# Kernel tuning notes

Measured on AMD Instinct MI355X. Metric: run time of the kernel, lower is better.

## Reference

```python
import jax, jax.numpy as jnp
import numpy as np

D_MODEL = 1024
NUM_HEADS = 16


def setup_inputs() -> dict:
    key = jax.random.key(0)
    kx, kq, kk, kv, ko = jax.random.split(key, 5)
    B, S, D = 4, 2048, D_MODEL
    scale = 0.02
    x = jax.random.normal(kx, (B, S, D), dtype=jnp.float32)
    wq = jax.random.normal(kq, (D, D), dtype=jnp.float32) * scale
    wk = jax.random.normal(kk, (D, D), dtype=jnp.float32) * scale
    wv = jax.random.normal(kv, (D, D), dtype=jnp.float32) * scale
    wo = jax.random.normal(ko, (D, D), dtype=jnp.float32) * scale
    return {"x": x, "wq": wq, "wk": wk, "wv": wv, "wo": wo}


def reference(x, wq, wk, wv, wo):
    B, S, D = x.shape
    H = NUM_HEADS
    dk = D // H
    # projections: weight is [out, in] -> y = x @ W^T
    q = jnp.einsum('bsd,ed->bse', x, wq).reshape(B, S, H, dk).transpose(0, 2, 1, 3)
    k = jnp.einsum('bsd,ed->bse', x, wk).reshape(B, S, H, dk).transpose(0, 2, 1, 3)
    v = jnp.einsum('bsd,ed->bse', x, wv).reshape(B, S, H, dk).transpose(0, 2, 1, 3)
    # scaled dot-product attention with causal mask, [B,H,S,S]
    scores = jnp.einsum('bhqd,bhkd->bhqk', q, k) / jnp.sqrt(jnp.asarray(dk, x.dtype))
    causal = jnp.tril(jnp.ones((S, S), dtype=bool))
    scores = jnp.where(causal, scores, -jnp.inf)
    attn = jax.nn.softmax(scores, axis=-1)
    out = jnp.einsum('bhqk,bhkd->bhqd', attn, v)
    out = out.transpose(0, 2, 1, 3).reshape(B, S, D)
    return jnp.einsum('bse,de->bsd', out, wo)
```

## Files before the change

### kernel.cpp

```cpp
#include <hip/hip_runtime.h>

#define SEQ 2048
#define DM 1024
#define NH 16
#define DKH 64

typedef __attribute__((ext_vector_type(8))) short short8;
typedef __attribute__((ext_vector_type(4))) float f32x4;

static __device__ __forceinline__ unsigned short f2b(float f) {
  unsigned int u = __float_as_uint(f);
  u += 0x7fffu + ((u >> 16) & 1u);
  return (unsigned short)(u >> 16);
}

static __device__ __forceinline__ short8 ldfrag_bf(const unsigned short* p) {
  return *reinterpret_cast<const short8*>(p);
}
static __device__ __forceinline__ short8 ldfrag_f32(const float* p) {
  const float4* q = reinterpret_cast<const float4*>(p);
  float4 a = q[0], b = q[1];
  short8 r;
  r[0] = (short)f2b(a.x); r[1] = (short)f2b(a.y);
  r[2] = (short)f2b(a.z); r[3] = (short)f2b(a.w);
  r[4] = (short)f2b(b.x); r[5] = (short)f2b(b.y);
  r[6] = (short)f2b(b.z); r[7] = (short)f2b(b.w);
  return r;
}

static __device__ __forceinline__ void gl_lds16(const void* g, void* l) {
  __builtin_amdgcn_global_load_lds(
      (const __attribute__((address_space(1))) unsigned int*)g,
      (__attribute__((address_space(3))) unsigned int*)l, 16, 0, 0);
}

__global__ __launch_bounds__(256) void zero_f32(float* __restrict__ p, int n4) {
  int i = blockIdx.x * 256 + threadIdx.x;
  if (i < n4) {
    float4 z = {0.f, 0.f, 0.f, 0.f};
    reinterpret_cast<float4*>(p)[i] = z;
  }
}

__global__ __launch_bounds__(256) void cast_f32_bf16(const float* __restrict__ src,
                                                     unsigned short* __restrict__ dst,
                                                     int n4) {
  int i = blockIdx.x * 256 + threadIdx.x;
  if (i < n4) {
    float4 v = reinterpret_cast<const float4*>(src)[i];
    ushort4 o;
    o.x = f2b(v.x); o.y = f2b(v.y); o.z = f2b(v.z); o.w = f2b(v.w);
    reinterpret_cast<ushort4*>(dst)[i] = o;
  }
}

__global__ __launch_bounds__(256) void cast4_w(const float* __restrict__ a, const float* __restrict__ b,
                                               const float* __restrict__ c, const float* __restrict__ d,
                                               unsigned short* __restrict__ oa, unsigned short* __restrict__ ob,
                                               unsigned short* __restrict__ oc, unsigned short* __restrict__ od) {
  int which = blockIdx.x >> 10;
  int i = (blockIdx.x & 1023) * 256 + threadIdx.x;
  const float* s = (which == 0) ? a : (which == 1) ? b : (which == 2) ? c : d;
  unsigned short* o = (which == 0) ? oa : (which == 1) ? ob : (which == 2) ? oc : od;
  float sc = (which == 0) ? 0.125f : 1.0f;
  float4 v = reinterpret_cast<const float4*>(s)[i];
  ushort4 u;
  u.x = f2b(v.x * sc); u.y = f2b(v.y * sc); u.z = f2b(v.z * sc); u.w = f2b(v.w * sc);
  reinterpret_cast<ushort4*>(o)[i] = u;
}

__global__ __launch_bounds__(256) void gemm_qkv(const unsigned short* __restrict__ A,
                                                const unsigned short* __restrict__ Wq,
                                                const unsigned short* __restrict__ Wk,
                                                const unsigned short* __restrict__ Wv,
                                                unsigned short* __restrict__ Qb,
                                                unsigned short* __restrict__ Kb,
                                                unsigned short* __restrict__ Vt) {
  __shared__ char smem[32768];
  unsigned short* At = (unsigned short*)smem;
  unsigned short* Wt = (unsigned short*)(smem + 16384);
  int t = threadIdx.x;
  int lane = t & 63;
  int w = t >> 6;
  int l16 = lane & 15, q4 = lane >> 4;
  int mode = blockIdx.x % 3;
  int bid = blockIdx.x / 3;
  int mt = bid >> 3, nt = bid & 7;
  int m0 = mt * 128, n0 = nt * 128;
  int mw = (w & 1) * 64, nw = (w >> 1) * 64;
  const unsigned short* W = (mode == 0) ? Wq : (mode == 1) ? Wk : Wv;

  const f32x4 zero4 = {0.f, 0.f, 0.f, 0.f};
  f32x4 acc[4][4];
#pragma unroll
  for (int mi = 0; mi < 4; ++mi)
#pragma unroll
    for (int nj = 0; nj < 4; ++nj) acc[mi][nj] = zero4;

  int rl0 = t >> 2, cp = t & 3;
  const unsigned short* ga0 = A + (long)(m0 + rl0) * DM + ((cp - rl0) & 3) * 8;
  const unsigned short* ga1 = A + (long)(m0 + rl0 + 64) * DM + ((cp - (rl0 + 64)) & 3) * 8;
  const unsigned short* gw0 = W + (long)(n0 + rl0) * DM + ((cp - rl0) & 3) * 8;
  const unsigned short* gw1 = W + (long)(n0 + rl0 + 64) * DM + ((cp - (rl0 + 64)) & 3) * 8;
  char* lA = (char*)At + t * 16;
  char* lW = (char*)Wt + t * 16;

  int aoff[4], woff[4];
#pragma unroll
  for (int mi = 0; mi < 4; ++mi) {
    int r = mw + mi * 16 + l16;
    aoff[mi] = r * 32 + ((q4 + r) & 3) * 8;
  }
#pragma unroll
  for (int nj = 0; nj < 4; ++nj) {
    int r = nw + nj * 16 + l16;
    woff[nj] = r * 32 + ((q4 + r) & 3) * 8;
  }

  gl_lds16(ga0, lA); gl_lds16(ga1, lA + 4096);
  gl_lds16(gw0, lW); gl_lds16(gw1, lW + 4096);

  for (int ks = 0; ks < 32; ++ks) {
    __syncthreads();
    if (ks + 1 < 32) {
      ga0 += 32; ga1 += 32; gw0 += 32; gw1 += 32;
      int bo = ((ks + 1) & 1) * 8192;
      gl_lds16(ga0, lA + bo); gl_lds16(ga1, lA + bo + 4096);
      gl_lds16(gw0, lW + bo); gl_lds16(gw1, lW + bo + 4096);
    }
    const unsigned short* Ab = At + (ks & 1) * 4096;
    const unsigned short* Wb = Wt + (ks & 1) * 4096;

    short8 af[4], wf[4];
#pragma unroll
    for (int mi = 0; mi < 4; ++mi) af[mi] = ldfrag_bf(Ab + aoff[mi]);
#pragma unroll
    for (int nj = 0; nj < 4; ++nj) wf[nj] = ldfrag_bf(Wb + woff[nj]);
#pragma unroll
    for (int mi = 0; mi < 4; ++mi)
#pragma unroll
      for (int nj = 0; nj < 4; ++nj)
        acc[mi][nj] = __builtin_amdgcn_mfma_f32_16x16x32_bf16(af[mi], wf[nj], acc[mi][nj], 0, 0, 0);
  }

  if (mode != 2) {
    unsigned short* o = (mode == 0) ? Qb : Kb;
#pragma unroll
    for (int mi = 0; mi < 4; ++mi)
#pragma unroll
      for (int nj = 0; nj < 4; ++nj)
#pragma unroll
        for (int r = 0; r < 4; ++r) {
          int m = m0 + mw + mi * 16 + q4 * 4 + r;
          int n = n0 + nw + nj * 16 + l16;
          int b = m >> 11, s = m & 2047;
          int h = n >> 6, d = n & 63;
          long bh = (long)(b * NH + h);
          o[(bh * SEQ + s) * DKH + d] = f2b(acc[mi][nj][r]);
        }
  } else {
    __syncthreads();
    unsigned short* vle = (unsigned short*)(smem + w * 8192);
    unsigned int* vle32 = (unsigned int*)vle;
#pragma unroll
    for (int nj = 0; nj < 4; ++nj) {
      int d = nj * 16 + l16;
      int k8 = (d & 7) * 8;
#pragma unroll
      for (int mi = 0; mi < 4; ++mi)
#pragma unroll
        for (int r = 0; r < 4; r += 2) {
          int s = mi * 16 + q4 * 4 + r;
          unsigned int pk = (unsigned int)f2b(acc[mi][nj][r]) |
                            ((unsigned int)f2b(acc[mi][nj][r + 1]) << 16);
          vle32[d * 32 + ((s ^ k8) >> 1)] = pk;
        }
    }
    __asm__ volatile("s_waitcnt lgkmcnt(0)" ::: "memory");
    int b = m0 >> 11;
    int h = (n0 + nw) >> 6;
    long bh = (long)(b * NH + h);
    int sbase = (m0 + mw) & 2047;
    int dr_lo = lane >> 3, c = lane & 7;
#pragma unroll
    for (int pass = 0; pass < 8; ++pass) {
      int dr = pass * 8 + dr_lo;
      int cc = c ^ (dr & 7);
      short8 vv = ldfrag_bf(vle + dr * 64 + cc * 8);
      *reinterpret_cast<short8*>(Vt + (bh * DKH + dr) * SEQ + sbase + c * 8) = vv;
    }
  }
}

__global__ __launch_bounds__(256) void gemm_o(const unsigned short* __restrict__ A,
                                              const unsigned short* __restrict__ W,
                                              float* __restrict__ outp) {
  __shared__ char smem[32768];
  unsigned short* At = (unsigned short*)smem;
  unsigned short* Wt = (unsigned short*)(smem + 16384);
  int t = threadIdx.x;
  int lane = t & 63;
  int w = t >> 6;
  int l16 = lane & 15, q4 = lane >> 4;
  int mt = blockIdx.x >> 3, nt = blockIdx.x & 7;
  int m0 = mt * 128, n0 = nt * 128;
  int mw = (w & 1) * 64, nw = (w >> 1) * 64;

  const f32x4 zero4 = {0.f, 0.f, 0.f, 0.f};
  f32x4 acc[4][4];
#pragma unroll
  for (int mi = 0; mi < 4; ++mi)
#pragma unroll
    for (int nj = 0; nj < 4; ++nj) acc[mi][nj] = zero4;

  int rl0 = t >> 2, cp = t & 3;
  int b0 = m0 >> 11;
  const unsigned short* ga0;
  const unsigned short* ga1;
  {
    int s0 = (m0 & 2047) + rl0;
    ga0 = A + (long)b0 * (NH * SEQ * DKH) + (long)s0 * DKH + ((cp - rl0) & 3) * 8;
    int s1 = (m0 & 2047) + rl0 + 64;
    ga1 = A + (long)b0 * (NH * SEQ * DKH) + (long)s1 * DKH + ((cp - (rl0 + 64)) & 3) * 8;
  }
  const unsigned short* gw0 = W + (long)(n0 + rl0) * DM + ((cp - rl0) & 3) * 8;
  const unsigned short* gw1 = W + (long)(n0 + rl0 + 64) * DM + ((cp - (rl0 + 64)) & 3) * 8;
  char* lA = (char*)At + t * 16;
  char* lW = (char*)Wt + t * 16;

  int aoff[4], woff[4];
#pragma unroll
  for (int mi = 0; mi < 4; ++mi) {
    int r = mw + mi * 16 + l16;
    aoff[mi] = r * 32 + ((q4 + r) & 3) * 8;
  }
#pragma unroll
  for (int nj = 0; nj < 4; ++nj) {
    int r = nw + nj * 16 + l16;
    woff[nj] = r * 32 + ((q4 + r) & 3) * 8;
  }

  gl_lds16(ga0, lA); gl_lds16(ga1, lA + 4096);
  gl_lds16(gw0, lW); gl_lds16(gw1, lW + 4096);

  for (int ks = 0; ks < 32; ++ks) {
    __syncthreads();
    if (ks + 1 < 32) {
      int adv = ((ks & 1) == 0) ? 32 : (SEQ * DKH - 32);
      ga0 += adv; ga1 += adv; gw0 += 32; gw1 += 32;
      int bo = ((ks + 1) & 1) * 8192;
      gl_lds16(ga0, lA + bo); gl_lds16(ga1, lA + bo + 4096);
      gl_lds16(gw0, lW + bo); gl_lds16(gw1, lW + bo + 4096);
    }
    const unsigned short* Ab = At + (ks & 1) * 4096;
    const unsigned short* Wb = Wt + (ks & 1) * 4096;

    short8 af[4], wf[4];
#pragma unroll
    for (int mi = 0; mi < 4; ++mi) af[mi] = ldfrag_bf(Ab + aoff[mi]);
#pragma unroll
    for (int nj = 0; nj < 4; ++nj) wf[nj] = ldfrag_bf(Wb + woff[nj]);
#pragma unroll
    for (int mi = 0; mi < 4; ++mi)
#pragma unroll
      for (int nj = 0; nj < 4; ++nj)
        acc[mi][nj] = __builtin_amdgcn_mfma_f32_16x16x32_bf16(af[mi], wf[nj], acc[mi][nj], 0, 0, 0);
  }

#pragma unroll
  for (int mi = 0; mi < 4; ++mi)
#pragma unroll
    for (int nj = 0; nj < 4; ++nj)
#pragma unroll
      for (int r = 0; r < 4; ++r) {
        int m = m0 + mw + mi * 16 + q4 * 4 + r;
        int n = n0 + nw + nj * 16 + l16;
        outp[(long)m * DM + n] = acc[mi][nj][r];
      }
}

template<int MODE, bool AF32, bool WF32>
__global__ __launch_bounds__(256) void gemm_s(const void* __restrict__ Ap,
                                              const void* __restrict__ Wp,
                                              void* __restrict__ outp) {
  int wid  = (blockIdx.x * 256 + threadIdx.x) >> 6;
  int lane = threadIdx.x & 63;
  int l16  = lane & 15, q4 = lane >> 4;
  int tn = wid & 15, tm = wid >> 4;
  int m0 = tm * 32, n0 = tn * 64;

  const float*          Af = (const float*)Ap;
  const unsigned short* Ab = (const unsigned short*)Ap;
  const float*          Wf = (const float*)Wp;
  const unsigned short* Wb = (const unsigned short*)Wp;

  const f32x4 zero4 = {0.f, 0.f, 0.f, 0.f};
  f32x4 acc[2][4];
#pragma unroll
  for (int mi = 0; mi < 2; ++mi)
#pragma unroll
    for (int j = 0; j < 4; ++j) acc[mi][j] = zero4;

  int wrow[4];
#pragma unroll
  for (int j = 0; j < 4; ++j) wrow[j] = (n0 + j * 16 + l16) * DM;
  int arow[2] = {0, 0};
  long abase[2] = {0, 0};
  if (MODE != 3) {
#pragma unroll
    for (int mi = 0; mi < 2; ++mi) arow[mi] = (m0 + mi * 16 + l16) * DM;
  } else {
    int b = m0 >> 11;
#pragma unroll
    for (int mi = 0; mi < 2; ++mi) {
      int srow = (m0 & 2047) + mi * 16 + l16;
      abase[mi] = (long)b * (NH * SEQ * DKH) + (long)srow * DKH;
    }
  }

#pragma unroll 2
  for (int ks = 0; ks < 32; ++ks) {
    int ko = ks * 32 + q4 * 8;
    short8 bfrag[4];
#pragma unroll
    for (int j = 0; j < 4; ++j) {
      if constexpr (WF32) bfrag[j] = ldfrag_f32(Wf + wrow[j] + ko);
      else                bfrag[j] = ldfrag_bf(Wb + wrow[j] + ko);
    }
    short8 afrag[2];
    if constexpr (MODE != 3) {
#pragma unroll
      for (int mi = 0; mi < 2; ++mi) {
        if constexpr (AF32) afrag[mi] = ldfrag_f32(Af + arow[mi] + ko);
        else                afrag[mi] = ldfrag_bf(Ab + arow[mi] + ko);
      }
    } else {
      int h = ko >> 6, e63 = ko & 63;
#pragma unroll
      for (int mi = 0; mi < 2; ++mi)
        afrag[mi] = ldfrag_bf(Ab + abase[mi] + (long)h * (SEQ * DKH) + e63);
    }
#pragma unroll
    for (int mi = 0; mi < 2; ++mi)
#pragma unroll
      for (int j = 0; j < 4; ++j)
        acc[mi][j] = __builtin_amdgcn_mfma_f32_16x16x32_bf16(afrag[mi], bfrag[j], acc[mi][j], 0, 0, 0);
  }

#pragma unroll
  for (int mi = 0; mi < 2; ++mi) {
#pragma unroll
    for (int j = 0; j < 4; ++j) {
#pragma unroll
      for (int r = 0; r < 4; ++r) {
        float v = acc[mi][j][r];
        int m = m0 + mi * 16 + q4 * 4 + r;
        int n = n0 + j * 16 + l16;
        if constexpr (MODE == 3) {
          reinterpret_cast<float*>(outp)[(long)m * DM + n] = v;
        } else {
          int b = m >> 11, s = m & 2047;
          int h = n >> 6, d = n & 63;
          long bh = (long)(b * NH + h);
          unsigned short* o = reinterpret_cast<unsigned short*>(outp);
          if constexpr (MODE == 0)      o[(bh * SEQ + s) * DKH + d] = f2b(v * 0.125f);
          else if constexpr (MODE == 1) o[(bh * SEQ + s) * DKH + d] = f2b(v);
          else                          o[(bh * DKH + d) * SEQ + s] = f2b(v);
        }
      }
    }
  }
}

#define PSTR 72
__global__ __launch_bounds__(256) void attn_k(const unsigned short* __restrict__ Kbuf,
                                              const unsigned short* __restrict__ Vt,
                                              const unsigned short* __restrict__ Qbuf,
                                              unsigned short* __restrict__ Obuf) {
  __shared__ unsigned short Kt[2][64 * 64];
  __shared__ unsigned short Vts[2][64 * 64];
  __shared__ unsigned short Pl[4][32 * PSTR];

  int t = threadIdx.x;
  int lane = t & 63;
  int w = t >> 6;
  int l16 = lane & 15, q4 = lane >> 4;
  int qb = 15 - (blockIdx.x >> 6);
  int bh = blockIdx.x & 63;
  int q0 = qb * 128;
  int qw0 = q0 + w * 32;

  const unsigned short* Qh = Qbuf + (long)bh * (SEQ * DKH);
  const unsigned short* Kh = Kbuf + (long)bh * (SEQ * DKH);
  const unsigned short* Vh = Vt   + (long)bh * (DKH * SEQ);
  unsigned short* pl = Pl[w];

  short8 qf[2][2];
#pragma unroll
  for (int mi = 0; mi < 2; ++mi)
#pragma unroll
    for (int c = 0; c < 2; ++c)
      qf[mi][c] = ldfrag_bf(Qh + (qw0 + mi * 16 + l16) * DKH + c * 32 + q4 * 8);

  short8 onef;
#pragma unroll
  for (int j = 0; j < 8; ++j) onef[j] = (short)0x3F80;

  const f32x4 zero4 = {0.f, 0.f, 0.f, 0.f};
  f32x4 om[2][4], lsum[2];
#pragma unroll
  for (int mi = 0; mi < 2; ++mi) {
    lsum[mi] = zero4;
#pragma unroll
    for (int c = 0; c < 4; ++c) om[mi][c] = zero4;
  }

  int koff[4][2], voff[4][2];
#pragma unroll
  for (int tt = 0; tt < 4; ++tt) {
    int kr = tt * 16 + l16;
#pragma unroll
    for (int c = 0; c < 2; ++c) koff[tt][c] = kr * 64 + ((c * 4 + q4 + kr) & 7) * 8;
  }
#pragma unroll
  for (int c = 0; c < 4; ++c) {
    int dr = c * 16 + l16;
#pragma unroll
    for (int half = 0; half < 2; ++half) voff[c][half] = dr * 64 + ((half * 4 + q4 + dr) & 7) * 8;
  }

  int rl0 = t >> 3, cp = t & 7;
  const unsigned short* kp0 = Kh + (long)rl0 * DKH + ((cp - rl0) & 7) * 8;
  const unsigned short* kp1 = Kh + (long)(rl0 + 32) * DKH + ((cp - (rl0 + 32)) & 7) * 8;
  const unsigned short* vp0 = Vh + (long)rl0 * SEQ + ((cp - rl0) & 7) * 8;
  const unsigned short* vp1 = Vh + (long)(rl0 + 32) * SEQ + ((cp - (rl0 + 32)) & 7) * 8;
  char* lK = (char*)Kt + t * 16;
  char* lV = (char*)Vts + t * 16;

  int nk = 2 * qb + 2;
  gl_lds16(kp0, lK); gl_lds16(kp1, lK + 4096);
  gl_lds16(vp0, lV); gl_lds16(vp1, lV + 4096);

  for (int it = 0; it < nk; ++it) {
    __syncthreads();
    if (it + 1 < nk) {
      kp0 += 64 * DKH; kp1 += 64 * DKH; vp0 += 64; vp1 += 64;
      int bo = ((it + 1) & 1) * 8192;
      gl_lds16(kp0, lK + bo); gl_lds16(kp1, lK + bo + 4096);
      gl_lds16(vp0, lV + bo); gl_lds16(vp1, lV + bo + 4096);
    }

    int k0 = it * 64;
    if (k0 <= qw0 + 31) {
      const unsigned short* KT = Kt[0] + (it & 1) * 4096;
      const unsigned short* VT = Vts[0] + (it & 1) * 4096;
      bool needmask = (k0 + 63 > qw0);

      f32x4 s[2][4];
#pragma unroll
      for (int mi = 0; mi < 2; ++mi)
#pragma unroll
        for (int tt = 0; tt < 4; ++tt) s[mi][tt] = zero4;
#pragma unroll
      for (int tt = 0; tt < 4; ++tt) {
#pragma unroll
        for (int c = 0; c < 2; ++c) {
          short8 kf = ldfrag_bf(KT + koff[tt][c]);
#pragma unroll
          for (int mi = 0; mi < 2; ++mi)
            s[mi][tt] = __builtin_amdgcn_mfma_f32_16x16x32_bf16(qf[mi][c], kf, s[mi][tt], 0, 0, 0);
        }
      }
#pragma unroll
      for (int mi = 0; mi < 2; ++mi)
#pragma unroll
        for (int tt = 0; tt < 4; ++tt) {
          int key = k0 + tt * 16 + l16;
#pragma unroll
          for (int r = 0; r < 4; ++r) {
            float p;
            if (needmask) {
              int qrow = qw0 + mi * 16 + q4 * 4 + r;
              p = (key <= qrow) ? __expf(s[mi][tt][r]) : 0.f;
            } else {
              p = __expf(s[mi][tt][r]);
            }
            pl[(mi * 16 + q4 * 4 + r) * PSTR + tt * 16 + l16] =
                (unsigned short)(__float_as_uint(p) >> 16);
          }
        }
      __asm__ volatile("s_waitcnt lgkmcnt(0)" ::: "memory");
#pragma unroll
      for (int half = 0; half < 2; ++half) {
        short8 pa[2];
#pragma unroll
        for (int mi = 0; mi < 2; ++mi) {
          pa[mi] = ldfrag_bf(pl + (mi * 16 + l16) * PSTR + half * 32 + q4 * 8);
          lsum[mi] = __builtin_amdgcn_mfma_f32_16x16x32_bf16(pa[mi], onef, lsum[mi], 0, 0, 0);
        }
#pragma unroll
        for (int c = 0; c < 4; ++c) {
          short8 vf = ldfrag_bf(VT + voff[c][half]);
#pragma unroll
          for (int mi = 0; mi < 2; ++mi)
            om[mi][c] = __builtin_amdgcn_mfma_f32_16x16x32_bf16(pa[mi], vf, om[mi][c], 0, 0, 0);
        }
      }
    }
  }

#pragma unroll
  for (int mi = 0; mi < 2; ++mi) {
    float inv[4];
#pragma unroll
    for (int r = 0; r < 4; ++r) inv[r] = 1.f / lsum[mi][r];
#pragma unroll
    for (int c = 0; c < 4; ++c)
#pragma unroll
      for (int r = 0; r < 4; ++r) {
        int row = qw0 + mi * 16 + q4 * 4 + r;
        Obuf[(long)bh * (SEQ * DKH) + row * DKH + c * 16 + l16] = f2b(om[mi][c][r] * inv[r]);
      }
  }
}

extern "C" void kernel_launch(void* const* d_in, const int* in_sizes, int n_in,
                              void* d_out, int out_size, void* d_ws, size_t ws_size,
                              hipStream_t stream) {
  const float* x  = (const float*)d_in[0];
  const float* wq = (const float*)d_in[1];
  const float* wk = (const float*)d_in[2];
  const float* wv = (const float*)d_in[3];
  const float* wo = (const float*)d_in[4];

  unsigned short* Qb = (unsigned short*)d_out;
  unsigned short* Kb = Qb + 8388608;

  if (ws_size >= 41943040ull) {
    unsigned short* xb  = (unsigned short*)d_ws;
    unsigned short* wqb = xb + 8388608;
    unsigned short* wkb = wqb + 1048576;
    unsigned short* wvb = wkb + 1048576;
    unsigned short* wob = wvb + 1048576;
    unsigned short* Vt  = wob + 1048576;
    unsigned short* Ob  = xb;

    cast_f32_bf16<<<8192, 256, 0, stream>>>(x, xb, 2097152);
    cast4_w<<<4096, 256, 0, stream>>>(wq, wk, wv, wo, wqb, wkb, wvb, wob);

    gemm_qkv<<<1536, 256, 0, stream>>>(xb, wqb, wkb, wvb, Qb, Kb, Vt);
    attn_k<<<1024, 256, 0, stream>>>(Kb, Vt, Qb, Ob);
    gemm_o<<<512, 256, 0, stream>>>(Ob, wob, (float*)d_out);
  } else if (ws_size >= 33554432ull) {
    unsigned short* Vt = (unsigned short*)d_ws;
    unsigned short* Ob = Vt + 8388608;

    gemm_s<0, true, true><<<1024, 256, 0, stream>>>(x, wq, Qb);
    gemm_s<1, true, true><<<1024, 256, 0, stream>>>(x, wk, Kb);
    gemm_s<2, true, true><<<1024, 256, 0, stream>>>(x, wv, Vt);
    attn_k<<<1024, 256, 0, stream>>>(Kb, Vt, Qb, Ob);
    gemm_s<3, false, true><<<1024, 256, 0, stream>>>(Ob, wo, d_out);
  } else {
    zero_f32<<<8192, 256, 0, stream>>>((float*)d_out, 2097152);
  }
}
```

Before: 273.8 us.

## Use 32x32 MFMA with transposed scores and register-resident P via permlane swap

Rewrites the attention inner loop to compute S^T with 32x32x16 bf16 MFMAs, so each lane holds scores for a single query row. This lets P be packed to bf16 in registers and rearranged with permlane32_swap instead of making a round trip through LDS. The row sum is now accumulated with scalar adds instead of an MFMA against a ones vector, and a 32-key sub-block skip refines the causal masking. It also drops the P shared buffer and adds a launch-bounds occupancy hint, at the cost of a more intricate lane/row mapping and shuffles in the epilogue.

```diff
diff --git a/kernel.cpp b/kernel.cpp
--- a/kernel.cpp
+++ b/kernel.cpp
@@ -7,6 +7,9 @@
 
 typedef __attribute__((ext_vector_type(8))) short short8;
 typedef __attribute__((ext_vector_type(4))) float f32x4;
+typedef __attribute__((ext_vector_type(16))) float f32x16;
+typedef __attribute__((ext_vector_type(2))) unsigned int u32x2;
+typedef __attribute__((ext_vector_type(4))) unsigned int u32x4;
 
 static __device__ __forceinline__ unsigned short f2b(float f) {
   unsigned int u = __float_as_uint(f);
@@ -372,19 +375,17 @@
   }
 }
 
-#define PSTR 72
-__global__ __launch_bounds__(256) void attn_k(const unsigned short* __restrict__ Kbuf,
-                                              const unsigned short* __restrict__ Vt,
-                                              const unsigned short* __restrict__ Qbuf,
-                                              unsigned short* __restrict__ Obuf) {
+__global__ __launch_bounds__(256, 4) void attn_k(const unsigned short* __restrict__ Kbuf,
+                                                 const unsigned short* __restrict__ Vt,
+                                                 const unsigned short* __restrict__ Qbuf,
+                                                 unsigned short* __restrict__ Obuf) {
   __shared__ unsigned short Kt[2][64 * 64];
   __shared__ unsigned short Vts[2][64 * 64];
-  __shared__ unsigned short Pl[4][32 * PSTR];
 
   int t = threadIdx.x;
   int lane = t & 63;
   int w = t >> 6;
-  int l16 = lane & 15, q4 = lane >> 4;
+  int l31 = lane & 31, hi = lane >> 5;
   int qb = 15 - (blockIdx.x >> 6);
   int bh = blockIdx.x & 63;
   int q0 = qb * 128;
@@ -393,40 +394,34 @@
   const unsigned short* Qh = Qbuf + (long)bh * (SEQ * DKH);
   const unsigned short* Kh = Kbuf + (long)bh * (SEQ * DKH);
   const unsigned short* Vh = Vt   + (long)bh * (DKH * SEQ);
-  unsigned short* pl = Pl[w];
-
-  short8 qf[2][2];
-#pragma unroll
-  for (int mi = 0; mi < 2; ++mi)
-#pragma unroll
-    for (int c = 0; c < 2; ++c)
-      qf[mi][c] = ldfrag_bf(Qh + (qw0 + mi * 16 + l16) * DKH + c * 32 + q4 * 8);
-
-  short8 onef;
-#pragma unroll
-  for (int j = 0; j < 8; ++j) onef[j] = (short)0x3F80;
-
-  const f32x4 zero4 = {0.f, 0.f, 0.f, 0.f};
-  f32x4 om[2][4], lsum[2];
-#pragma unroll
-  for (int mi = 0; mi < 2; ++mi) {
-    lsum[mi] = zero4;
-#pragma unroll
-    for (int c = 0; c < 4; ++c) om[mi][c] = zero4;
-  }
-
-  int koff[4][2], voff[4][2];
-#pragma unroll
-  for (int tt = 0; tt < 4; ++tt) {
-    int kr = tt * 16 + l16;
-#pragma unroll
-    for (int c = 0; c < 2; ++c) koff[tt][c] = kr * 64 + ((c * 4 + q4 + kr) & 7) * 8;
-  }
-#pragma unroll
-  for (int c = 0; c < 4; ++c) {
-    int dr = c * 16 + l16;
-#pragma unroll
-    for (int half = 0; half < 2; ++half) voff[c][half] = dr * 64 + ((half * 4 + q4 + dr) & 7) * 8;
+
+  short8 qf[4];
+#pragma unroll
+  for (int dt = 0; dt < 4; ++dt)
+    qf[dt] = ldfrag_bf(Qh + (long)(qw0 + l31) * DKH + dt * 16 + hi * 8);
+
+  f32x16 om[2];
+#pragma unroll
+  for (int dv = 0; dv < 2; ++dv)
+#pragma unroll
+    for (int r = 0; r < 16; ++r) om[dv][r] = 0.f;
+  float lsum = 0.f;
+
+  int koff[2][4];
+#pragma unroll
+  for (int sub = 0; sub < 2; ++sub) {
+    int kr = sub * 32 + l31;
+#pragma unroll
+    for (int dt = 0; dt < 4; ++dt)
+      koff[sub][dt] = kr * 64 + ((dt * 2 + hi + kr) & 7) * 8;
+  }
+  int voff[2][4];
+#pragma unroll
+  for (int dv = 0; dv < 2; ++dv) {
+    int dr = dv * 32 + l31;
+#pragma unroll
+    for (int kc = 0; kc < 4; ++kc)
+      voff[dv][kc] = dr * 64 + ((kc * 2 + hi + dr) & 7) * 8;
   }
 
   int rl0 = t >> 3, cp = t & 7;
@@ -454,73 +449,69 @@
     if (k0 <= qw0 + 31) {
       const unsigned short* KT = Kt[0] + (it & 1) * 4096;
       const unsigned short* VT = Vts[0] + (it & 1) * 4096;
-      bool needmask = (k0 + 63 > qw0);
-
-      f32x4 s[2][4];
-#pragma unroll
-      for (int mi = 0; mi < 2; ++mi)
-#pragma unroll
-        for (int tt = 0; tt < 4; ++tt) s[mi][tt] = zero4;
-#pragma unroll
-      for (int tt = 0; tt < 4; ++tt) {
-#pragma unroll
-        for (int c = 0; c < 2; ++c) {
-          short8 kf = ldfrag_bf(KT + koff[tt][c]);
-#pragma unroll
-          for (int mi = 0; mi < 2; ++mi)
-            s[mi][tt] = __builtin_amdgcn_mfma_f32_16x16x32_bf16(qf[mi][c], kf, s[mi][tt], 0, 0, 0);
+
+#pragma unroll
+      for (int sub = 0; sub < 2; ++sub) {
+        int ksb = k0 + sub * 32;
+        if (ksb <= qw0 + 31) {
+          f32x16 s;
+#pragma unroll
+          for (int r = 0; r < 16; ++r) s[r] = 0.f;
+#pragma unroll
+          for (int dt = 0; dt < 4; ++dt) {
+            short8 kf = ldfrag_bf(KT + koff[sub][dt]);
+            s = __builtin_amdgcn_mfma_f32_32x32x16_bf16(kf, qf[dt], s, 0, 0, 0);
+          }
+
+          bool needmask = (ksb + 31 > qw0);
+          int qr = qw0 + l31;
+          unsigned int pk[4][2];
+#pragma unroll
+          for (int r = 0; r < 16; r += 2) {
+            float p0 = __expf(s[r]);
+            float p1 = __expf(s[r + 1]);
+            if (needmask) {
+              int key = ksb + (r & 3) + 8 * (r >> 2) + 4 * hi;
+              p0 = (key <= qr) ? p0 : 0.f;
+              p1 = (key + 1 <= qr) ? p1 : 0.f;
+            }
+            unsigned int u0 = __float_as_uint(p0) & 0xffff0000u;
+            unsigned int u1 = __float_as_uint(p1) & 0xffff0000u;
+            lsum += __uint_as_float(u0) + __uint_as_float(u1);
+            pk[r >> 2][(r >> 1) & 1] = (u0 >> 16) | u1;
+          }
+
+#pragma unroll
+          for (int c = 0; c < 2; ++c) {
+            u32x2 r0 = __builtin_amdgcn_permlane32_swap(pk[2 * c][0], pk[2 * c + 1][0], false, false);
+            u32x2 r1 = __builtin_amdgcn_permlane32_swap(pk[2 * c][1], pk[2 * c + 1][1], false, false);
+            u32x4 pw;
+            pw.x = r0.x; pw.y = r1.x; pw.z = r0.y; pw.w = r1.y;
+            short8 pa = __builtin_bit_cast(short8, pw);
+            int kc = sub * 2 + c;
+#pragma unroll
+            for (int dv = 0; dv < 2; ++dv) {
+              short8 vf = ldfrag_bf(VT + voff[dv][kc]);
+              om[dv] = __builtin_amdgcn_mfma_f32_32x32x16_bf16(pa, vf, om[dv], 0, 0, 0);
+            }
+          }
         }
       }
-#pragma unroll
-      for (int mi = 0; mi < 2; ++mi)
-#pragma unroll
-        for (int tt = 0; tt < 4; ++tt) {
-          int key = k0 + tt * 16 + l16;
-#pragma unroll
-          for (int r = 0; r < 4; ++r) {
-            float p;
-            if (needmask) {
-              int qrow = qw0 + mi * 16 + q4 * 4 + r;
-              p = (key <= qrow) ? __expf(s[mi][tt][r]) : 0.f;
-            } else {
-              p = __expf(s[mi][tt][r]);
-            }
-            pl[(mi * 16 + q4 * 4 + r) * PSTR + tt * 16 + l16] =
-                (unsigned short)(__float_as_uint(p) >> 16);
-          }
-        }
-      __asm__ volatile("s_waitcnt lgkmcnt(0)" ::: "memory");
-#pragma unroll
-      for (int half = 0; half < 2; ++half) {
-        short8 pa[2];
-#pragma unroll
-        for (int mi = 0; mi < 2; ++mi) {
-          pa[mi] = ldfrag_bf(pl + (mi * 16 + l16) * PSTR + half * 32 + q4 * 8);
-          lsum[mi] = __builtin_amdgcn_mfma_f32_16x16x32_bf16(pa[mi], onef, lsum[mi], 0, 0, 0);
-        }
-#pragma unroll
-        for (int c = 0; c < 4; ++c) {
-          short8 vf = ldfrag_bf(VT + voff[c][half]);
-#pragma unroll
-          for (int mi = 0; mi < 2; ++mi)
-            om[mi][c] = __builtin_amdgcn_mfma_f32_16x16x32_bf16(pa[mi], vf, om[mi][c], 0, 0, 0);
-        }
-      }
-    }
-  }
-
-#pragma unroll
-  for (int mi = 0; mi < 2; ++mi) {
-    float inv[4];
-#pragma unroll
-    for (int r = 0; r < 4; ++r) inv[r] = 1.f / lsum[mi][r];
-#pragma unroll
-    for (int c = 0; c < 4; ++c)
-#pragma unroll
-      for (int r = 0; r < 4; ++r) {
-        int row = qw0 + mi * 16 + q4 * 4 + r;
-        Obuf[(long)bh * (SEQ * DKH) + row * DKH + c * 16 + l16] = f2b(om[mi][c][r] * inv[r]);
-      }
+    }
+  }
+
+  u32x2 lz = __builtin_amdgcn_permlane32_swap(__float_as_uint(lsum), __float_as_uint(lsum),
+                                              false, false);
+  float inv = 1.f / (__uint_as_float(lz.x) + __uint_as_float(lz.y));
+
+  long obase = (long)bh * (SEQ * DKH);
+#pragma unroll
+  for (int r = 0; r < 16; ++r) {
+    int qrow = (r & 3) + 8 * (r >> 2) + 4 * hi;
+    float invq = __shfl(inv, qrow);
+    long rowb = obase + (long)(qw0 + qrow) * DKH + l31;
+    Obuf[rowb]      = f2b(om[0][r] * invq);
+    Obuf[rowb + 32] = f2b(om[1][r] * invq);
   }
 }
 
```

New measurement: 255.3 us. 6.8% less time.
